# Performance work log

Hardware: AMD Instinct MI355X
Metric: run time of the kernel (lower is better)

The kernel has to match this reference:

```python
import jax, jax.numpy as jnp
import numpy as np

B, S, D, H = 4, 2048, 1024, 16
HD = D // H


def setup_inputs() -> dict:
    key = jax.random.key(0)
    k1, k2, k3 = jax.random.split(key, 3)
    hidden_states = jax.random.normal(k1, (B, S, D), dtype=jnp.float32)
    # torch nn.Linear weights: [out_features, in_features], no bias
    w_qkv = jax.random.normal(k2, (3 * D, D), dtype=jnp.float32) * (D ** -0.5)
    w_out = jax.random.normal(k3, (D, D), dtype=jnp.float32) * (D ** -0.5)
    attention_mask = jnp.ones((B, S), dtype=bool)  # True = attend
    # causal mask: True = masked (strict upper triangle)
    causal_mask = jnp.triu(jnp.ones((S, S), dtype=bool), k=1)[None, None, :, :]
    return {
        "hidden_states": hidden_states,
        "w_qkv": w_qkv,
        "w_out": w_out,
        "attention_mask": attention_mask,
        "causal_mask": causal_mask,
    }


def reference(hidden_states, w_qkv, w_out, attention_mask, causal_mask):
    b, s, d = hidden_states.shape
    scale = HD ** -0.5
    qkv = hidden_states @ w_qkv.T                      # [B,S,3D]
    qkv = qkv.reshape(b, s, 3, H, HD)
    qkv = jnp.transpose(qkv, (2, 0, 3, 1, 4))          # [3,B,H,S,HD]
    q, k, v = qkv[0], qkv[1], qkv[2]
    scores = jnp.einsum("bhqd,bhkd->bhqk", q, k) * scale
    scores = jnp.where(causal_mask, -jnp.inf, scores)
    key_mask = ~attention_mask[:, None, None, :]       # [B,1,1,S], True = masked
    scores = jnp.where(key_mask, -jnp.inf, scores)
    attn = jax.nn.softmax(scores, axis=-1)             # dropout: eval mode (identity)
    out = jnp.einsum("bhqk,bhkd->bhqd", attn, v)       # [B,H,S,HD]
    out = jnp.transpose(out, (0, 2, 1, 3)).reshape(b, s, d)
    return out @ w_out.T
```

## Files before the change

### kernel.cpp

```cpp
#include <hip/hip_runtime.h>

#define B_ 4
#define S_ 2048
#define D_ 1024
#define H_ 16
#define HD_ 64
#define QKV_LD (3*D_)
#define NEG_BIG (-1e30f)
#define PSCALE 0.18033688f
#define PSHIFT 11.5415603f

typedef __bf16 bf16x8 __attribute__((ext_vector_type(8)));
typedef float f32x4 __attribute__((ext_vector_type(4)));

__device__ __forceinline__ unsigned short f2bf(float f) {
    union { float f; unsigned int u; } v; v.f = f;
    return (unsigned short)((v.u + 0x8000u) >> 16);
}

__device__ __forceinline__ unsigned pack_bf(float a, float b) {
    union { float f; unsigned u; } x, y; x.f = a; y.f = b;
    return __builtin_amdgcn_perm(y.u + 0x8000u, x.u + 0x8000u, 0x07060302u);
}

__device__ __forceinline__ void glds16(const unsigned short* g, unsigned short* l) {
    __builtin_amdgcn_global_load_lds(
        (const __attribute__((address_space(1))) unsigned int*)g,
        (__attribute__((address_space(3))) unsigned int*)l, 16, 0, 0);
}

__global__ __launch_bounds__(256) void cvt_bf16(const float* __restrict__ src,
                                                unsigned short* __restrict__ dst, int n8) {
    int i = blockIdx.x * 256 + threadIdx.x;
    if (i < n8) {
        const float4 f0 = *(const float4*)(src + (size_t)i * 8);
        const float4 f1 = *(const float4*)(src + (size_t)i * 8 + 4);
        uint4 o;
        o.x = pack_bf(f0.x, f0.y); o.y = pack_bf(f0.z, f0.w);
        o.z = pack_bf(f1.x, f1.y); o.w = pack_bf(f1.z, f1.w);
        *(uint4*)(dst + (size_t)i * 8) = o;
    }
}

template<int CF32>
__global__ __launch_bounds__(256) void gemm_lds(const unsigned short* __restrict__ A,
                                                const unsigned short* __restrict__ W,
                                                void* __restrict__ Cp,
                                                int M, int N, int K)
{
    __shared__ unsigned short As[128*32];
    __shared__ unsigned short Bs[128*32];
    const int tid  = threadIdx.x;
    const int wave = tid >> 6, lane = tid & 63;
    const int l15 = lane & 15, l4 = lane >> 4;
    const int m0 = blockIdx.y * 128, n0 = blockIdx.x * 128;
    const int wr = (wave >> 1) * 64, wc = (wave & 1) * 64;

    const f32x4 fzero = {0.f, 0.f, 0.f, 0.f};
    f32x4 acc[4][4];
    #pragma unroll
    for (int i = 0; i < 4; ++i)
        #pragma unroll
        for (int j = 0; j < 4; ++j) acc[i][j] = fzero;

    const unsigned short* Ab = A + (size_t)(m0 + wave*32 + (lane >> 2)) * K + (lane & 3) * 8;
    const unsigned short* Wb = W + (size_t)(n0 + wave*32 + (lane >> 2)) * K + (lane & 3) * 8;
    unsigned short* AsW = &As[wave * 32 * 32];
    unsigned short* BsW = &Bs[wave * 32 * 32];
    const size_t K16 = (size_t)16 * K;

    for (int k0 = 0; k0 < K; k0 += 32) {
        __syncthreads();
        glds16(Ab + k0,       AsW);
        glds16(Ab + K16 + k0, AsW + 16*32);
        glds16(Wb + k0,       BsW);
        glds16(Wb + K16 + k0, BsW + 16*32);
        __syncthreads();
        bf16x8 af[4], bfr[4];
        #pragma unroll
        for (int mi = 0; mi < 4; ++mi)
            af[mi] = *(const bf16x8*)&As[(wr + mi*16 + l15) * 32 + l4 * 8];
        #pragma unroll
        for (int ni = 0; ni < 4; ++ni)
            bfr[ni] = *(const bf16x8*)&Bs[(wc + ni*16 + l15) * 32 + l4 * 8];
        #pragma unroll
        for (int mi = 0; mi < 4; ++mi)
            #pragma unroll
            for (int ni = 0; ni < 4; ++ni)
                acc[mi][ni] = __builtin_amdgcn_mfma_f32_16x16x32_bf16(af[mi], bfr[ni], acc[mi][ni], 0, 0, 0);
    }

    #pragma unroll
    for (int mi = 0; mi < 4; ++mi)
        #pragma unroll
        for (int ni = 0; ni < 4; ++ni)
            #pragma unroll
            for (int r = 0; r < 4; ++r) {
                int m = m0 + wr + mi*16 + l4*4 + r;
                int n = n0 + wc + ni*16 + l15;
                if (CF32) ((float*)Cp)[(size_t)m * N + n] = acc[mi][ni][r];
                else      ((unsigned short*)Cp)[(size_t)m * N + n] = f2bf(acc[mi][ni][r]);
            }
}

__global__ __launch_bounds__(256) void attn_fwd(const unsigned short* __restrict__ qkv,
                                                unsigned short* __restrict__ out)
{
    __shared__ unsigned short Qs [128*72];
    __shared__ unsigned short Ks [64*72];
    __shared__ unsigned short Vts[64*72];
    unsigned short (*Ps)[32*72] = reinterpret_cast<unsigned short(*)[32*72]>(Qs);

    const int tid  = threadIdx.x;
    const int wave = tid >> 6, lane = tid & 63;
    const int l15 = lane & 15, l4 = lane >> 4;
    const int qb = 15 - blockIdx.y;
    const int bh = blockIdx.x;
    const int b = bh >> 4, h = bh & 15;
    const int q0 = qb * 128;

    const unsigned short* Qg = qkv + (size_t)b * S_ * QKV_LD + h * HD_;
    const unsigned short* Kg = Qg + D_;
    const unsigned short* Vg = Qg + 2 * D_;

    #pragma unroll
    for (int i = 0; i < 4; ++i) {
        int lin = i * 256 + tid;
        int r = lin >> 3, c = (lin & 7) * 8;
        *(uint4*)&Qs[r * 72 + c] = *(const uint4*)&Qg[(size_t)(q0 + r) * QKV_LD + c];
    }
    __syncthreads();
    bf16x8 aq[2][2];
    #pragma unroll
    for (int mi = 0; mi < 2; ++mi)
        #pragma unroll
        for (int hf = 0; hf < 2; ++hf)
            aq[mi][hf] = *(const bf16x8*)&Qs[(wave*32 + mi*16 + l15) * 72 + hf*32 + l4 * 8];

    const f32x4 fzero = {0.f, 0.f, 0.f, 0.f};
    f32x4 oacc[2][4];
    float l_i[2][4];
    #pragma unroll
    for (int mi = 0; mi < 2; ++mi)
        #pragma unroll
        for (int x = 0; x < 4; ++x) { oacc[mi][x] = fzero; l_i[mi][x] = 0.f; }

    const int kr = tid >> 3, kc = (tid & 7) * 8;
    const int vr = tid >> 2, vc0 = (tid & 3) * 16;
    const int vcolp = (vr + vc0) & 63;
    const int wq0 = q0 + wave * 32;
    const int jmax = 2 * qb + 1;

    uint4 kq0 = *(const uint4*)&Kg[(size_t)kr * QKV_LD + kc];
    uint4 kq1 = *(const uint4*)&Kg[(size_t)(32 + kr) * QKV_LD + kc];
    uint4 vq0 = *(const uint4*)&Vg[(size_t)vr * QKV_LD + vc0];
    uint4 vq1 = *(const uint4*)&Vg[(size_t)vr * QKV_LD + vc0 + 8];

    for (int j = 0; j <= jmax; ++j) {
        __syncthreads();
        *(uint4*)&Ks[kr * 72 + kc]        = kq0;
        *(uint4*)&Ks[(32 + kr) * 72 + kc] = kq1;
        {
            union { uint4 q[2]; unsigned short u[16]; } tmp;
            tmp.q[0] = vq0; tmp.q[1] = vq1;
            #pragma unroll
            for (int i = 0; i < 16; ++i) Vts[(vc0 + i) * 72 + vcolp] = tmp.u[i];
        }
        __syncthreads();

        if (j < jmax) {
            const size_t k0n = (size_t)(j + 1) * 64;
            kq0 = *(const uint4*)&Kg[(k0n + kr) * QKV_LD + kc];
            kq1 = *(const uint4*)&Kg[(k0n + 32 + kr) * QKV_LD + kc];
            vq0 = *(const uint4*)&Vg[(k0n + vr) * QKV_LD + vc0];
            vq1 = *(const uint4*)&Vg[(k0n + vr) * QKV_LD + vc0 + 8];
        }

        if (64 * j < wq0 + 32) {
            f32x4 sfr[2][4];
            #pragma unroll
            for (int ni = 0; ni < 4; ++ni) {
                bf16x8 kb0 = *(const bf16x8*)&Ks[(ni*16 + l15) * 72 + l4 * 8];
                bf16x8 kb1 = *(const bf16x8*)&Ks[(ni*16 + l15) * 72 + 32 + l4 * 8];
                #pragma unroll
                for (int mi = 0; mi < 2; ++mi) {
                    f32x4 a = fzero;
                    a = __builtin_amdgcn_mfma_f32_16x16x32_bf16(aq[mi][0], kb0, a, 0, 0, 0);
                    a = __builtin_amdgcn_mfma_f32_16x16x32_bf16(aq[mi][1], kb1, a, 0, 0, 0);
                    sfr[mi][ni] = a;
                }
            }
            if (64 * (j + 1) > wq0) {
                const int off = wq0 - 64 * j;
                #pragma unroll
                for (int mi = 0; mi < 2; ++mi)
                    #pragma unroll
                    for (int ni = 0; ni < 4; ++ni)
                        #pragma unroll
                        for (int r = 0; r < 4; ++r)
                            if (ni*16 + l15 > off + mi*16 + l4*4 + r) sfr[mi][ni][r] = NEG_BIG;
            }
            #pragma unroll
            for (int mi = 0; mi < 2; ++mi)
                #pragma unroll
                for (int ni = 0; ni < 4; ++ni)
                    #pragma unroll
                    for (int r = 0; r < 4; ++r) {
                        float p = __builtin_exp2f(sfr[mi][ni][r] * PSCALE - PSHIFT);
                        sfr[mi][ni][r] = p;
                        Ps[wave][(mi*16 + l4*4 + r) * 72 + ((ni*16 + l15 + l4*16) & 63)] = f2bf(p);
                    }
            #pragma unroll
            for (int mi = 0; mi < 2; ++mi)
                #pragma unroll
                for (int r = 0; r < 4; ++r)
                    l_i[mi][r] += (sfr[mi][0][r] + sfr[mi][1][r]) + (sfr[mi][2][r] + sfr[mi][3][r]);

            asm volatile("s_waitcnt lgkmcnt(0)" ::: "memory");

            #pragma unroll
            for (int ks = 0; ks < 2; ++ks) {
                bf16x8 ap[2];
                #pragma unroll
                for (int mi = 0; mi < 2; ++mi)
                    ap[mi] = *(const bf16x8*)&Ps[wave][(mi*16 + l15) * 72 + ((ks*32 + l4*8 + (l15 >> 2)*16) & 63)];
                #pragma unroll
                for (int ni = 0; ni < 4; ++ni) {
                    bf16x8 bv = *(const bf16x8*)&Vts[(ni*16 + l15) * 72 + ((ks*32 + l4*8 + ni*16) & 63)];
                    #pragma unroll
                    for (int mi = 0; mi < 2; ++mi)
                        oacc[mi][ni] = __builtin_amdgcn_mfma_f32_16x16x32_bf16(ap[mi], bv, oacc[mi][ni], 0, 0, 0);
                }
            }
        }
    }

    #pragma unroll
    for (int mi = 0; mi < 2; ++mi)
        #pragma unroll
        for (int r = 0; r < 4; ++r) {
            float s = l_i[mi][r];
            #pragma unroll
            for (int msk = 1; msk <= 8; msk <<= 1)
                s += __shfl_xor(s, msk);
            float inv = (s > 0.f) ? (1.0f / s) : 0.f;
            int q = q0 + wave*32 + mi*16 + l4*4 + r;
            size_t base = ((size_t)b * S_ + q) * D_ + h * HD_;
            #pragma unroll
            for (int ni = 0; ni < 4; ++ni)
                out[base + ni*16 + l15] = f2bf(oacc[mi][ni][r] * inv);
        }
}

extern "C" void kernel_launch(void* const* d_in, const int* in_sizes, int n_in,
                              void* d_out, int out_size, void* d_ws, size_t ws_size,
                              hipStream_t stream)
{
    const float* hidden = (const float*)d_in[0];
    const float* w_qkv  = (const float*)d_in[1];
    const float* w_out  = (const float*)d_in[2];

    const int M = B_ * S_;

    unsigned short* qkv_ws  = (unsigned short*)d_ws;
    unsigned short* attn_ws = qkv_ws + (size_t)M * 3 * D_;
    unsigned short* Hb = attn_ws;
    unsigned short* Wq = (unsigned short*)d_out;
    unsigned short* Wo = qkv_ws;

    cvt_bf16<<<(M*D_/8 + 255)/256,      256, 0, stream>>>(hidden, Hb, M*D_/8);
    cvt_bf16<<<(3*D_*D_/8 + 255)/256,   256, 0, stream>>>(w_qkv,  Wq, 3*D_*D_/8);
    gemm_lds<0><<<dim3(3*D_/128, M/128), 256, 0, stream>>>(Hb, Wq, qkv_ws, M, 3*D_, D_);
    attn_fwd<<<dim3(B_*H_, S_/128), 256, 0, stream>>>(qkv_ws, attn_ws);
    cvt_bf16<<<(D_*D_/8 + 255)/256,     256, 0, stream>>>(w_out, Wo, D_*D_/8);
    gemm_lds<1><<<dim3(D_/128, M/128), 256, 0, stream>>>(attn_ws, Wo, d_out, M, D_, D_);
}
```

Measured before the change: 301.7 us.

## Pair causal query blocks per workgroup and double-buffer K/V tiles

Each workgroup now processes two query blocks (a long and a short one from opposite ends of the causal triangle), halving the grid and equalizing per-block work. K and V shared tiles are double-buffered so the next tile is written while the current one is consumed, reducing barriers per iteration to one. This raises LDS usage and may reduce the number of resident blocks per CU and overall parallelism.

```diff
diff --git a/kernel.cpp b/kernel.cpp
--- a/kernel.cpp
+++ b/kernel.cpp
@@ -107,149 +107,164 @@
                                                 unsigned short* __restrict__ out)
 {
     __shared__ unsigned short Qs [128*72];
-    __shared__ unsigned short Ks [64*72];
-    __shared__ unsigned short Vts[64*72];
+    __shared__ unsigned short Ks [2][64*72];
+    __shared__ unsigned short Vts[2][64*72];
     unsigned short (*Ps)[32*72] = reinterpret_cast<unsigned short(*)[32*72]>(Qs);
 
     const int tid  = threadIdx.x;
     const int wave = tid >> 6, lane = tid & 63;
     const int l15 = lane & 15, l4 = lane >> 4;
-    const int qb = 15 - blockIdx.y;
     const int bh = blockIdx.x;
     const int b = bh >> 4, h = bh & 15;
-    const int q0 = qb * 128;
 
     const unsigned short* Qg = qkv + (size_t)b * S_ * QKV_LD + h * HD_;
     const unsigned short* Kg = Qg + D_;
     const unsigned short* Vg = Qg + 2 * D_;
 
-    #pragma unroll
-    for (int i = 0; i < 4; ++i) {
-        int lin = i * 256 + tid;
-        int r = lin >> 3, c = (lin & 7) * 8;
-        *(uint4*)&Qs[r * 72 + c] = *(const uint4*)&Qg[(size_t)(q0 + r) * QKV_LD + c];
-    }
-    __syncthreads();
-    bf16x8 aq[2][2];
-    #pragma unroll
-    for (int mi = 0; mi < 2; ++mi)
-        #pragma unroll
-        for (int hf = 0; hf < 2; ++hf)
-            aq[mi][hf] = *(const bf16x8*)&Qs[(wave*32 + mi*16 + l15) * 72 + hf*32 + l4 * 8];
-
-    const f32x4 fzero = {0.f, 0.f, 0.f, 0.f};
-    f32x4 oacc[2][4];
-    float l_i[2][4];
-    #pragma unroll
-    for (int mi = 0; mi < 2; ++mi)
-        #pragma unroll
-        for (int x = 0; x < 4; ++x) { oacc[mi][x] = fzero; l_i[mi][x] = 0.f; }
-
     const int kr = tid >> 3, kc = (tid & 7) * 8;
     const int vr = tid >> 2, vc0 = (tid & 3) * 16;
     const int vcolp = (vr + vc0) & 63;
-    const int wq0 = q0 + wave * 32;
-    const int jmax = 2 * qb + 1;
-
-    uint4 kq0 = *(const uint4*)&Kg[(size_t)kr * QKV_LD + kc];
-    uint4 kq1 = *(const uint4*)&Kg[(size_t)(32 + kr) * QKV_LD + kc];
-    uint4 vq0 = *(const uint4*)&Vg[(size_t)vr * QKV_LD + vc0];
-    uint4 vq1 = *(const uint4*)&Vg[(size_t)vr * QKV_LD + vc0 + 8];
-
-    for (int j = 0; j <= jmax; ++j) {
-        __syncthreads();
-        *(uint4*)&Ks[kr * 72 + kc]        = kq0;
-        *(uint4*)&Ks[(32 + kr) * 72 + kc] = kq1;
+    const f32x4 fzero = {0.f, 0.f, 0.f, 0.f};
+
+    for (int half = 0; half < 2; ++half) {
+        const int qb = half ? (int)blockIdx.y : 15 - (int)blockIdx.y;
+        const int q0 = qb * 128;
+        const int wq0 = q0 + wave * 32;
+        const int jmax = 2 * qb + 1;
+
+        #pragma unroll
+        for (int i = 0; i < 4; ++i) {
+            int lin = i * 256 + tid;
+            int r = lin >> 3, c = (lin & 7) * 8;
+            *(uint4*)&Qs[r * 72 + c] = *(const uint4*)&Qg[(size_t)(q0 + r) * QKV_LD + c];
+        }
+        __syncthreads();
+        bf16x8 aq[2][2];
+        #pragma unroll
+        for (int mi = 0; mi < 2; ++mi)
+            #pragma unroll
+            for (int hf = 0; hf < 2; ++hf)
+                aq[mi][hf] = *(const bf16x8*)&Qs[(wave*32 + mi*16 + l15) * 72 + hf*32 + l4 * 8];
+
+        f32x4 oacc[2][4];
+        float l_i[2][4];
+        #pragma unroll
+        for (int mi = 0; mi < 2; ++mi)
+            #pragma unroll
+            for (int x = 0; x < 4; ++x) { oacc[mi][x] = fzero; l_i[mi][x] = 0.f; }
+
+        uint4 kq0 = *(const uint4*)&Kg[(size_t)kr * QKV_LD + kc];
+        uint4 kq1 = *(const uint4*)&Kg[(size_t)(32 + kr) * QKV_LD + kc];
+        uint4 vq0 = *(const uint4*)&Vg[(size_t)vr * QKV_LD + vc0];
+        uint4 vq1 = *(const uint4*)&Vg[(size_t)vr * QKV_LD + vc0 + 8];
+        *(uint4*)&Ks[0][kr * 72 + kc]        = kq0;
+        *(uint4*)&Ks[0][(32 + kr) * 72 + kc] = kq1;
         {
             union { uint4 q[2]; unsigned short u[16]; } tmp;
             tmp.q[0] = vq0; tmp.q[1] = vq1;
             #pragma unroll
-            for (int i = 0; i < 16; ++i) Vts[(vc0 + i) * 72 + vcolp] = tmp.u[i];
+            for (int i = 0; i < 16; ++i) Vts[0][(vc0 + i) * 72 + vcolp] = tmp.u[i];
         }
-        __syncthreads();
-
-        if (j < jmax) {
-            const size_t k0n = (size_t)(j + 1) * 64;
-            kq0 = *(const uint4*)&Kg[(k0n + kr) * QKV_LD + kc];
-            kq1 = *(const uint4*)&Kg[(k0n + 32 + kr) * QKV_LD + kc];
-            vq0 = *(const uint4*)&Vg[(k0n + vr) * QKV_LD + vc0];
-            vq1 = *(const uint4*)&Vg[(k0n + vr) * QKV_LD + vc0 + 8];
-        }
-
-        if (64 * j < wq0 + 32) {
-            f32x4 sfr[2][4];
-            #pragma unroll
-            for (int ni = 0; ni < 4; ++ni) {
-                bf16x8 kb0 = *(const bf16x8*)&Ks[(ni*16 + l15) * 72 + l4 * 8];
-                bf16x8 kb1 = *(const bf16x8*)&Ks[(ni*16 + l15) * 72 + 32 + l4 * 8];
-                #pragma unroll
-                for (int mi = 0; mi < 2; ++mi) {
-                    f32x4 a = fzero;
-                    a = __builtin_amdgcn_mfma_f32_16x16x32_bf16(aq[mi][0], kb0, a, 0, 0, 0);
-                    a = __builtin_amdgcn_mfma_f32_16x16x32_bf16(aq[mi][1], kb1, a, 0, 0, 0);
-                    sfr[mi][ni] = a;
+        kq0 = *(const uint4*)&Kg[(size_t)(64 + kr) * QKV_LD + kc];
+        kq1 = *(const uint4*)&Kg[(size_t)(96 + kr) * QKV_LD + kc];
+        vq0 = *(const uint4*)&Vg[(size_t)(64 + vr) * QKV_LD + vc0];
+        vq1 = *(const uint4*)&Vg[(size_t)(64 + vr) * QKV_LD + vc0 + 8];
+        __syncthreads();
+
+        for (int j = 0; j <= jmax; ++j) {
+            const int cur = j & 1, nxt = cur ^ 1;
+            if (j < jmax) {
+                *(uint4*)&Ks[nxt][kr * 72 + kc]        = kq0;
+                *(uint4*)&Ks[nxt][(32 + kr) * 72 + kc] = kq1;
+                union { uint4 q[2]; unsigned short u[16]; } tmp;
+                tmp.q[0] = vq0; tmp.q[1] = vq1;
+                #pragma unroll
+                for (int i = 0; i < 16; ++i) Vts[nxt][(vc0 + i) * 72 + vcolp] = tmp.u[i];
+            }
+            if (j + 2 <= jmax) {
+                const size_t k0n = (size_t)(j + 2) * 64;
+                kq0 = *(const uint4*)&Kg[(k0n + kr) * QKV_LD + kc];
+                kq1 = *(const uint4*)&Kg[(k0n + 32 + kr) * QKV_LD + kc];
+                vq0 = *(const uint4*)&Vg[(k0n + vr) * QKV_LD + vc0];
+                vq1 = *(const uint4*)&Vg[(k0n + vr) * QKV_LD + vc0 + 8];
+            }
+
+            if (64 * j < wq0 + 32) {
+                f32x4 sfr[2][4];
+                #pragma unroll
+                for (int ni = 0; ni < 4; ++ni) {
+                    bf16x8 kb0 = *(const bf16x8*)&Ks[cur][(ni*16 + l15) * 72 + l4 * 8];
+                    bf16x8 kb1 = *(const bf16x8*)&Ks[cur][(ni*16 + l15) * 72 + 32 + l4 * 8];
+                    #pragma unroll
+                    for (int mi = 0; mi < 2; ++mi) {
+                        f32x4 a = fzero;
+                        a = __builtin_amdgcn_mfma_f32_16x16x32_bf16(aq[mi][0], kb0, a, 0, 0, 0);
+                        a = __builtin_amdgcn_mfma_f32_16x16x32_bf16(aq[mi][1], kb1, a, 0, 0, 0);
+                        sfr[mi][ni] = a;
+                    }
                 }
-            }
-            if (64 * (j + 1) > wq0) {
-                const int off = wq0 - 64 * j;
+                if (64 * (j + 1) > wq0) {
+                    const int off = wq0 - 64 * j;
+                    #pragma unroll
+                    for (int mi = 0; mi < 2; ++mi)
+                        #pragma unroll
+                        for (int ni = 0; ni < 4; ++ni)
+                            #pragma unroll
+                            for (int r = 0; r < 4; ++r)
+                                if (ni*16 + l15 > off + mi*16 + l4*4 + r) sfr[mi][ni][r] = NEG_BIG;
+                }
                 #pragma unroll
                 for (int mi = 0; mi < 2; ++mi)
                     #pragma unroll
                     for (int ni = 0; ni < 4; ++ni)
                         #pragma unroll
-                        for (int r = 0; r < 4; ++r)
-                            if (ni*16 + l15 > off + mi*16 + l4*4 + r) sfr[mi][ni][r] = NEG_BIG;
-            }
-            #pragma unroll
-            for (int mi = 0; mi < 2; ++mi)
+                        for (int r = 0; r < 4; ++r) {
+                            float p = __builtin_exp2f(sfr[mi][ni][r] * PSCALE - PSHIFT);
+                            sfr[mi][ni][r] = p;
+                            Ps[wave][(mi*16 + l4*4 + r) * 72 + ((ni*16 + l15 + l4*16) & 63)] = f2bf(p);
+                        }
+                #pragma unroll
+                for (int mi = 0; mi < 2; ++mi)
+                    #pragma unroll
+                    for (int r = 0; r < 4; ++r)
+                        l_i[mi][r] += (sfr[mi][0][r] + sfr[mi][1][r]) + (sfr[mi][2][r] + sfr[mi][3][r]);
+
+                asm volatile("s_waitcnt lgkmcnt(0)" ::: "memory");
+
+                #pragma unroll
+                for (int ks = 0; ks < 2; ++ks) {
+                    bf16x8 ap[2];
+                    #pragma unroll
+                    for (int mi = 0; mi < 2; ++mi)
+                        ap[mi] = *(const bf16x8*)&Ps[wave][(mi*16 + l15) * 72 + ((ks*32 + l4*8 + (l15 >> 2)*16) & 63)];
+                    #pragma unroll
+                    for (int ni = 0; ni < 4; ++ni) {
+                        bf16x8 bv = *(const bf16x8*)&Vts[cur][(ni*16 + l15) * 72 + ((ks*32 + l4*8 + ni*16) & 63)];
+                        #pragma unroll
+                        for (int mi = 0; mi < 2; ++mi)
+                            oacc[mi][ni] = __builtin_amdgcn_mfma_f32_16x16x32_bf16(ap[mi], bv, oacc[mi][ni], 0, 0, 0);
+                    }
+                }
+            }
+            __syncthreads();
+        }
+
+        #pragma unroll
+        for (int mi = 0; mi < 2; ++mi)
+            #pragma unroll
+            for (int r = 0; r < 4; ++r) {
+                float s = l_i[mi][r];
+                #pragma unroll
+                for (int msk = 1; msk <= 8; msk <<= 1)
+                    s += __shfl_xor(s, msk);
+                float inv = (s > 0.f) ? (1.0f / s) : 0.f;
+                int q = q0 + wave*32 + mi*16 + l4*4 + r;
+                size_t base = ((size_t)b * S_ + q) * D_ + h * HD_;
                 #pragma unroll
                 for (int ni = 0; ni < 4; ++ni)
-                    #pragma unroll
-                    for (int r = 0; r < 4; ++r) {
-                        float p = __builtin_exp2f(sfr[mi][ni][r] * PSCALE - PSHIFT);
-                        sfr[mi][ni][r] = p;
-                        Ps[wave][(mi*16 + l4*4 + r) * 72 + ((ni*16 + l15 + l4*16) & 63)] = f2bf(p);
-                    }
-            #pragma unroll
-            for (int mi = 0; mi < 2; ++mi)
-                #pragma unroll
-                for (int r = 0; r < 4; ++r)
-                    l_i[mi][r] += (sfr[mi][0][r] + sfr[mi][1][r]) + (sfr[mi][2][r] + sfr[mi][3][r]);
-
-            asm volatile("s_waitcnt lgkmcnt(0)" ::: "memory");
-
-            #pragma unroll
-            for (int ks = 0; ks < 2; ++ks) {
-                bf16x8 ap[2];
-                #pragma unroll
-                for (int mi = 0; mi < 2; ++mi)
-                    ap[mi] = *(const bf16x8*)&Ps[wave][(mi*16 + l15) * 72 + ((ks*32 + l4*8 + (l15 >> 2)*16) & 63)];
-                #pragma unroll
-                for (int ni = 0; ni < 4; ++ni) {
-                    bf16x8 bv = *(const bf16x8*)&Vts[(ni*16 + l15) * 72 + ((ks*32 + l4*8 + ni*16) & 63)];
-                    #pragma unroll
-                    for (int mi = 0; mi < 2; ++mi)
-                        oacc[mi][ni] = __builtin_amdgcn_mfma_f32_16x16x32_bf16(ap[mi], bv, oacc[mi][ni], 0, 0, 0);
-                }
-            }
-        }
+                    out[base + ni*16 + l15] = f2bf(oacc[mi][ni][r] * inv);
+            }
     }
-
-    #pragma unroll
-    for (int mi = 0; mi < 2; ++mi)
-        #pragma unroll
-        for (int r = 0; r < 4; ++r) {
-            float s = l_i[mi][r];
-            #pragma unroll
-            for (int msk = 1; msk <= 8; msk <<= 1)
-                s += __shfl_xor(s, msk);
-            float inv = (s > 0.f) ? (1.0f / s) : 0.f;
-            int q = q0 + wave*32 + mi*16 + l4*4 + r;
-            size_t base = ((size_t)b * S_ + q) * D_ + h * HD_;
-            #pragma unroll
-            for (int ni = 0; ni < 4; ++ni)
-                out[base + ni*16 + l15] = f2bf(oacc[mi][ni][r] * inv);
-        }
 }
 
 extern "C" void kernel_launch(void* const* d_in, const int* in_sizes, int n_in,
@@ -271,7 +286,7 @@
     cvt_bf16<<<(M*D_/8 + 255)/256,      256, 0, stream>>>(hidden, Hb, M*D_/8);
     cvt_bf16<<<(3*D_*D_/8 + 255)/256,   256, 0, stream>>>(w_qkv,  Wq, 3*D_*D_/8);
     gemm_lds<0><<<dim3(3*D_/128, M/128), 256, 0, stream>>>(Hb, Wq, qkv_ws, M, 3*D_, D_);
-    attn_fwd<<<dim3(B_*H_, S_/128), 256, 0, stream>>>(qkv_ws, attn_ws);
+    attn_fwd<<<dim3(B_*H_, 8), 256, 0, stream>>>(qkv_ws, attn_ws);
     cvt_bf16<<<(D_*D_/8 + 255)/256,     256, 0, stream>>>(w_out, Wo, D_*D_/8);
     gemm_lds<1><<<dim3(D_/128, M/128), 256, 0, stream>>>(attn_ws, Wo, d_out, M, D_, D_);
 }
```

Measured after the change: 309.4 us. 2.6% more time.
